# Kernel tuning notes

Measured on AMD Instinct MI355X. Metric: run time of the kernel, lower is better.

## Reference

```python
import jax, jax.numpy as jnp
import numpy as np

B, S, D, H, DFF = 2, 2048, 1024, 16, 4096
DK = D // H
EPS = 1e-5

def setup_inputs() -> dict:
    key = jax.random.key(0)
    ks = jax.random.split(key, 8)
    sc = lambda n: 1.0 / np.sqrt(n)
    return {
        "x": jax.random.normal(ks[0], (B, S, D), dtype=jnp.float32),
        "g1": jnp.ones((D,), dtype=jnp.float32),
        "g2": jnp.ones((D,), dtype=jnp.float32),
        "wq": jax.random.normal(ks[1], (D, D), dtype=jnp.float32) * sc(D),
        "wk": jax.random.normal(ks[2], (D, D), dtype=jnp.float32) * sc(D),
        "wv": jax.random.normal(ks[3], (D, D), dtype=jnp.float32) * sc(D),
        "wo": jax.random.normal(ks[4], (D, D), dtype=jnp.float32) * sc(D),
        "w1": jax.random.normal(ks[5], (DFF, D), dtype=jnp.float32) * sc(D),
        "w2": jax.random.normal(ks[6], (D, DFF), dtype=jnp.float32) * sc(DFF),
    }

def rmsnorm(a, g):
    norm = jnp.sqrt(jnp.mean(a * a, axis=-1, keepdims=True) + EPS)
    return a / norm * g

def gelu_erf(x):
    return x * 0.5 * (1.0 + jax.lax.erf(x * (1.0 / np.sqrt(2.0))))

def reference(x, g1, g2, wq, wk, wv, wo, w1, w2):
    b, s, d = x.shape
    h, dk = H, DK
    # --- attention sublayer (pre-norm) ---
    xn = rmsnorm(x, g1)
    # nn.Linear: y = x @ W.T ; reshape to [b, h, s, dk]
    q = (xn @ wq.T).reshape(b, s, h, dk).transpose(0, 2, 1, 3)
    k = (xn @ wk.T).reshape(b, s, h, dk).transpose(0, 2, 1, 3)
    v = (xn @ wv.T).reshape(b, s, h, dk).transpose(0, 2, 1, 3)
    scores = jnp.einsum('bhqd,bhkd->bhqk', q, k) / np.sqrt(dk).astype(np.float32)
    causal = jnp.triu(jnp.ones((s, s), dtype=bool), k=1)  # True above diagonal -> masked
    scores = jnp.where(causal, -jnp.inf, scores)
    weights = jax.nn.softmax(scores, axis=-1)
    attn = jnp.einsum('bhqk,bhkd->bhqd', weights, v)
    attn = attn.transpose(0, 2, 1, 3).reshape(b, s, d)
    x = x + attn @ wo.T
    # --- FFN sublayer (pre-norm) ---
    xn2 = rmsnorm(x, g2)
    ff = gelu_erf(xn2 @ w1.T) @ w2.T
    return x + ff
```

## Files before the change

### kernel.cpp

```cpp
#include <hip/hip_runtime.h>
#include <hip/hip_bf16.h>

typedef __attribute__((ext_vector_type(8))) short bf16x8;
typedef __attribute__((ext_vector_type(4))) float f32x4;

__device__ __forceinline__ unsigned short f2b(float f) {
    unsigned int u = __float_as_uint(f);
    unsigned int r = u + 0x7FFFu + ((u >> 16) & 1u);
    return (unsigned short)(r >> 16);
}

__device__ __forceinline__ float gelu_erf(float v) {
    return 0.5f * v * (1.0f + erff(v * 0.70710678118654752f));
}

__device__ __forceinline__ void gload_lds16(const void* g, void* l) {
    __builtin_amdgcn_global_load_lds(
        (const __attribute__((address_space(1))) void*)g,
        (__attribute__((address_space(3))) void*)l, 16, 0, 0);
}

__global__ void cast_all_k(const float* __restrict__ wq, const float* __restrict__ wk,
                           const float* __restrict__ wv, const float* __restrict__ wo,
                           const float* __restrict__ w1, const float* __restrict__ w2,
                           unsigned short* __restrict__ wqkv_b, unsigned short* __restrict__ wo_b,
                           unsigned short* __restrict__ w1_b, unsigned short* __restrict__ w2_b,
                           float qscale) {
    const int S = 262144, F = 1048576;
    int i = blockIdx.x * blockDim.x + threadIdx.x;
    const float* src; unsigned short* dst; int off; float scale = 1.0f;
    if (i < S)              { src = wq; dst = wqkv_b;             off = i;          scale = qscale; }
    else if (i < 2 * S)     { src = wk; dst = wqkv_b + S * 4;     off = i - S; }
    else if (i < 3 * S)     { src = wv; dst = wqkv_b + 2 * S * 4; off = i - 2 * S; }
    else if (i < 4 * S)     { src = wo; dst = wo_b;               off = i - 3 * S; }
    else if (i < 4 * S + F) { src = w1; dst = w1_b;               off = i - 4 * S; }
    else                    { src = w2; dst = w2_b;               off = i - 4 * S - F; }
    float4 v = ((const float4*)src)[off];
    ushort4 o;
    o.x = f2b(v.x * scale); o.y = f2b(v.y * scale);
    o.z = f2b(v.z * scale); o.w = f2b(v.w * scale);
    ((ushort4*)(dst))[off] = o;
}

__global__ void rmsnorm_bf16_k(const float* __restrict__ x, const float* __restrict__ g,
                               unsigned short* __restrict__ out) {
    int row = blockIdx.x;
    int t = threadIdx.x;
    const float4* xr = (const float4*)(x + (size_t)row * 1024);
    float4 xv = xr[t];
    float ss = xv.x * xv.x + xv.y * xv.y + xv.z * xv.z + xv.w * xv.w;
    #pragma unroll
    for (int off = 32; off; off >>= 1) ss += __shfl_xor(ss, off, 64);
    __shared__ float red[4];
    int wave = t >> 6, lane = t & 63;
    if (lane == 0) red[wave] = ss;
    __syncthreads();
    float tot = red[0] + red[1] + red[2] + red[3];
    float rn = rsqrtf(tot * (1.0f / 1024.0f) + 1e-5f);
    float4 gv = ((const float4*)g)[t];
    ushort4 o4;
    o4.x = f2b(xv.x * rn * gv.x);
    o4.y = f2b(xv.y * rn * gv.y);
    o4.z = f2b(xv.z * rn * gv.z);
    o4.w = f2b(xv.w * rn * gv.w);
    ((ushort4*)out)[(size_t)row * 256 + t] = o4;
}

__global__ void vtrans_k(const unsigned short* __restrict__ qkv, unsigned short* __restrict__ vt) {
    __shared__ unsigned short Ls[64 * 72];
    int st = blockIdx.x, bh = blockIdx.y, b = bh >> 4, h = bh & 15;
    int s0 = st * 64;
    int tid = threadIdx.x;
    const unsigned short* Vg = qkv + (size_t)(b * 2048 + s0) * 3072 + 2048 + h * 64;
    #pragma unroll
    for (int i = 0; i < 2; i++) {
        int idx = i * 256 + tid;
        int r = idx >> 3, c8 = (idx & 7) * 8;
        *(uint4*)&Ls[r * 72 + c8] = *(const uint4*)&Vg[(size_t)r * 3072 + c8];
    }
    __syncthreads();
    #pragma unroll
    for (int i = 0; i < 2; i++) {
        int idx = i * 256 + tid;
        int d = idx >> 3, s8 = (idx & 7) * 8;
        unsigned short tmp[8];
        #pragma unroll
        for (int j = 0; j < 8; j++) tmp[j] = Ls[(s8 + j) * 72 + d];
        *(uint4*)&vt[(size_t)(bh * 64 + d) * 2048 + s0 + s8] = *(uint4*)tmp;
    }
}

template <int EPI>
__launch_bounds__(256)
__global__ void gemm_bt(const unsigned short* __restrict__ A, const unsigned short* __restrict__ B,
                        const float* __restrict__ res, void* __restrict__ out,
                        int M, int N, int K) {
    __shared__ __align__(16) unsigned short smem[2 * 128 * 32];
    unsigned short* As = smem;
    unsigned short* Bs = smem + 128 * 32;

    int tid = threadIdx.x;
    int wave = tid >> 6, lane = tid & 63;
    int lrow = lane & 15, quad = lane >> 4;
    int qx8 = (quad ^ ((lrow >> 1) & 3)) * 8;

    int gx = gridDim.x, gy = gridDim.y;
    int cid = blockIdx.y * gx + blockIdx.x;
    int per = (gx * gy) >> 3;
    int nid = (cid & 7) * per + (cid >> 3);
    const int CG = 8;
    int group = nid / (CG * gy);
    int rem = nid % (CG * gy);
    int bxs = group * CG + (rem % CG);
    int bys = rem / CG;
    int bm = bys * 128, bn = bxs * 128;

    int wm = (wave & 1) * 64, wn = (wave >> 1) * 64;

    const unsigned short* Ab = A + (size_t)bm * K;
    const unsigned short* Bb = B + (size_t)bn * K;

    f32x4 zero = {0.f, 0.f, 0.f, 0.f};
    f32x4 acc[4][4];
    #pragma unroll
    for (int mi = 0; mi < 4; mi++)
        #pragma unroll
        for (int ni = 0; ni < 4; ni++) acc[mi][ni] = zero;

    int wbase = tid & 192;

    for (int k0 = 0; k0 < K; k0 += 32) {
        if (k0) __syncthreads();
        #pragma unroll
        for (int i = 0; i < 2; i++) {
            int idx = i * 256 + tid;
            int r = idx >> 2;
            int c = ((idx & 3) ^ ((idx >> 3) & 3)) * 8;
            gload_lds16(&Ab[(size_t)r * K + k0 + c], As + ((size_t)(i * 256 + wbase)) * 8);
            gload_lds16(&Bb[(size_t)r * K + k0 + c], Bs + ((size_t)(i * 256 + wbase)) * 8);
        }
        __syncthreads();

        bf16x8 af[4], bfr[4];
        #pragma unroll
        for (int mi = 0; mi < 4; mi++)
            af[mi] = *(const bf16x8*)&As[(wm + mi * 16 + lrow) * 32 + qx8];
        #pragma unroll
        for (int ni = 0; ni < 4; ni++)
            bfr[ni] = *(const bf16x8*)&Bs[(wn + ni * 16 + lrow) * 32 + qx8];
        #pragma unroll
        for (int mi = 0; mi < 4; mi++)
            #pragma unroll
            for (int ni = 0; ni < 4; ni++)
                acc[mi][ni] = __builtin_amdgcn_mfma_f32_16x16x32_bf16(af[mi], bfr[ni], acc[mi][ni], 0, 0, 0);
    }

    float* Cs = (float*)smem;
    int row16 = lane >> 2, cseg = (lane & 3) * 16;
    #pragma unroll
    for (int p = 0; p < 4; p++) {
        __syncthreads();
        #pragma unroll
        for (int ni = 0; ni < 4; ni++)
            #pragma unroll
            for (int r = 0; r < 4; r++)
                Cs[wave * 1024 + (quad * 4 + r) * 64 + ni * 16 + lrow] = acc[p][ni][r];
        __syncthreads();
        const float* src = &Cs[wave * 1024 + row16 * 64 + cseg];
        int grow = bm + wm + p * 16 + row16;
        int gcol = bn + wn + cseg;
        size_t off = (size_t)grow * N + gcol;
        if (EPI == 1) {
            float* op = (float*)out + off;
            const float* rp = res + off;
            #pragma unroll
            for (int j = 0; j < 4; j++) {
                float4 v = ((const float4*)src)[j];
                float4 rr = ((const float4*)rp)[j];
                v.x += rr.x; v.y += rr.y; v.z += rr.z; v.w += rr.w;
                ((float4*)op)[j] = v;
            }
        } else {
            unsigned short tmp[16];
            #pragma unroll
            for (int j = 0; j < 16; j++) {
                float v = src[j];
                if (EPI == 2) v = gelu_erf(v);
                tmp[j] = f2b(v);
            }
            unsigned short* op = (unsigned short*)out + off;
            *(uint4*)op = *(uint4*)tmp;
            *(uint4*)(op + 8) = *(uint4*)(tmp + 8);
        }
    }
}

__launch_bounds__(256)
__global__ void gemm_bt64(const unsigned short* __restrict__ A, const unsigned short* __restrict__ B,
                          const float* __restrict__ res, float* __restrict__ out,
                          int M, int N, int K) {
    __shared__ __align__(16) unsigned short As[2][128 * 32];
    __shared__ __align__(16) unsigned short Bs[2][64 * 32];

    int tid = threadIdx.x, wave = tid >> 6, lane = tid & 63;
    int lrow = lane & 15, quad = lane >> 4;
    int qx8 = (quad ^ ((lrow >> 1) & 3)) * 8;

    int gx = gridDim.x, gy = gridDim.y;
    int cid = blockIdx.y * gx + blockIdx.x;
    int per = (gx * gy) >> 3;
    int nid = (cid & 7) * per + (cid >> 3);
    const int CG = 8;
    int group = nid / (CG * gy);
    int rem = nid % (CG * gy);
    int bxs = group * CG + (rem % CG);
    int bys = rem / CG;
    int bm = bys * 128, bn = bxs * 64;

    int wm = (wave & 1) * 64, wn = (wave >> 1) * 32;

    f32x4 zero = {0.f, 0.f, 0.f, 0.f};
    f32x4 acc[4][2];
    #pragma unroll
    for (int mi = 0; mi < 4; mi++)
        #pragma unroll
        for (int ni = 0; ni < 2; ni++) acc[mi][ni] = zero;

    int rr4 = lane >> 2;
    int c8s = ((lane & 3) ^ ((lane >> 3) & 3)) * 8;
    const unsigned short* Ab = A + (size_t)(bm + wave * 32 + rr4) * K + c8s;
    const unsigned short* Bb = B + (size_t)(bn + wave * 16 + rr4) * K + c8s;

    auto stage = [&](int k0, int nb) {
        gload_lds16(Ab + k0, &As[nb][(wave * 32) * 32]);
        gload_lds16(Ab + (size_t)16 * K + k0, &As[nb][(wave * 32 + 16) * 32]);
        gload_lds16(Bb + k0, &Bs[nb][(wave * 16) * 32]);
    };

    int nIter = K >> 5;
    stage(0, 0);
    for (int it = 0; it < nIter; it++) {
        __syncthreads();
        if (it + 1 < nIter) stage((it + 1) * 32, (it + 1) & 1);
        int buf = it & 1;

        bf16x8 af[4], bfr[2];
        #pragma unroll
        for (int mi = 0; mi < 4; mi++)
            af[mi] = *(const bf16x8*)&As[buf][(wm + mi * 16 + lrow) * 32 + qx8];
        #pragma unroll
        for (int ni = 0; ni < 2; ni++)
            bfr[ni] = *(const bf16x8*)&Bs[buf][(wn + ni * 16 + lrow) * 32 + qx8];
        #pragma unroll
        for (int mi = 0; mi < 4; mi++)
            #pragma unroll
            for (int ni = 0; ni < 2; ni++)
                acc[mi][ni] = __builtin_amdgcn_mfma_f32_16x16x32_bf16(af[mi], bfr[ni], acc[mi][ni], 0, 0, 0);
    }

    float* Cs = (float*)As[0];
    int row16 = lane >> 2, cseg = (lane & 3) * 8;
    #pragma unroll
    for (int p = 0; p < 4; p++) {
        __syncthreads();
        #pragma unroll
        for (int ni = 0; ni < 2; ni++)
            #pragma unroll
            for (int r = 0; r < 4; r++)
                Cs[wave * 512 + (quad * 4 + r) * 32 + ni * 16 + lrow] = acc[p][ni][r];
        __syncthreads();
        const float* src = &Cs[wave * 512 + row16 * 32 + cseg];
        int grow = bm + wm + p * 16 + row16;
        int gcol = bn + wn + cseg;
        size_t off = (size_t)grow * N + gcol;
        float* op = out + off;
        const float* rp = res + off;
        #pragma unroll
        for (int j = 0; j < 2; j++) {
            float4 v = ((const float4*)src)[j];
            float4 rv = ((const float4*)rp)[j];
            v.x += rv.x; v.y += rv.y; v.z += rv.z; v.w += rv.w;
            ((float4*)op)[j] = v;
        }
    }
}

__launch_bounds__(256)
__global__ void attn_k(const unsigned short* __restrict__ qkv,
                       const unsigned short* __restrict__ vt,
                       unsigned short* __restrict__ attn_out) {
    const int ROWQKV = 3072;
    int cid = (int)(blockIdx.y * gridDim.x + blockIdx.x);
    int bh = (cid & 7) * 4 + (cid >> 6);
    int bx = (cid >> 3) & 7;
    int b = bh >> 4, h = bh & 15;
    int qtA = bx, qtB = 15 - bx;
    int nktA = 2 * qtA + 2, nktB = 2 * qtB + 2;
    int ntot = nktA + nktB;

    __shared__ __align__(16) unsigned short Ks[2][2][64 * 32];
    __shared__ __align__(16) unsigned short Vs[2][2][64 * 32];
    __shared__ __align__(16) unsigned short Ps[8][16 * 72];

    int tid = threadIdx.x, wave = tid >> 6, lane = tid & 63;
    int lrow = lane & 15, quad = lane >> 4;
    int rr4 = lane >> 2;
    int c8s = ((lane & 3) ^ ((lane >> 3) & 3)) * 8;
    int qx8 = (quad ^ ((lrow >> 1) & 3)) * 8;

    size_t base = (size_t)b * 2048 * ROWQKV;

    bf16x8 qf[2][2][2];
    #pragma unroll
    for (int p = 0; p < 2; p++) {
        int q0 = (p ? qtB : qtA) * 128;
        #pragma unroll
        for (int s = 0; s < 2; s++) {
            const unsigned short* Qg = qkv + base +
                (size_t)(q0 + s * 64 + wave * 16 + lrow) * ROWQKV + h * 64 + quad * 8;
            qf[p][s][0] = *(const bf16x8*)Qg;
            qf[p][s][1] = *(const bf16x8*)(Qg + 32);
        }
    }

    const unsigned short* Kg0 = qkv + base + (size_t)(wave * 16 + rr4) * ROWQKV + 1024 + h * 64 + c8s;
    const unsigned short* Vg0 = vt + (size_t)(bh * 64 + wave * 16 + rr4) * 2048 + c8s;

    auto stage = [&](int t, int nb) {
        const unsigned short* Kg = Kg0 + (size_t)(t * 64) * ROWQKV;
        const unsigned short* Vg = Vg0 + t * 64;
        gload_lds16(Kg,      &Ks[nb][0][wave * 16 * 32]);
        gload_lds16(Kg + 32, &Ks[nb][1][wave * 16 * 32]);
        gload_lds16(Vg,      &Vs[nb][0][wave * 16 * 32]);
        gload_lds16(Vg + 32, &Vs[nb][1][wave * 16 * 32]);
    };

    f32x4 zero = {0.f, 0.f, 0.f, 0.f};
    f32x4 oA[4], oB[4];
    float lA = 0.f, lB = 0.f;
    #pragma unroll
    for (int ni = 0; ni < 4; ni++) { oA[ni] = zero; oB[ni] = zero; }

    int qloc = wave * 16 + lrow;

    auto process = [&](bf16x8 q0f, bf16x8 q1f, f32x4* o, float& l,
                       unsigned short* Pw, bool diag, int buf) {
        f32x4 s[4];
        #pragma unroll
        for (int ni = 0; ni < 4; ni++) s[ni] = zero;
        #pragma unroll
        for (int ni = 0; ni < 4; ni++) {
            bf16x8 kf = *(const bf16x8*)&Ks[buf][0][(ni * 16 + lrow) * 32 + qx8];
            s[ni] = __builtin_amdgcn_mfma_f32_16x16x32_bf16(kf, q0f, s[ni], 0, 0, 0);
        }
        #pragma unroll
        for (int ni = 0; ni < 4; ni++) {
            bf16x8 kf = *(const bf16x8*)&Ks[buf][1][(ni * 16 + lrow) * 32 + qx8];
            s[ni] = __builtin_amdgcn_mfma_f32_16x16x32_bf16(kf, q1f, s[ni], 0, 0, 0);
        }
        if (diag) {
            #pragma unroll
            for (int ni = 0; ni < 4; ni++)
                #pragma unroll
                for (int r = 0; r < 4; r++) {
                    float p = exp2f(s[ni][r]);
                    if (ni * 16 + quad * 4 + r > qloc) p = 0.f;
                    s[ni][r] = p;
                    l += p;
                }
        } else {
            #pragma unroll
            for (int ni = 0; ni < 4; ni++)
                #pragma unroll
                for (int r = 0; r < 4; r++) {
                    float p = exp2f(s[ni][r]);
                    s[ni][r] = p;
                    l += p;
                }
        }
        #pragma unroll
        for (int ni = 0; ni < 4; ni++) {
            uint2 pk;
            pk.x = (unsigned int)f2b(s[ni][0]) | ((unsigned int)f2b(s[ni][1]) << 16);
            pk.y = (unsigned int)f2b(s[ni][2]) | ((unsigned int)f2b(s[ni][3]) << 16);
            *(uint2*)&Pw[lrow * 72 + ni * 16 + quad * 4] = pk;
        }
        bf16x8 p0 = *(const bf16x8*)&Pw[lrow * 72 + quad * 8];
        bf16x8 p1 = *(const bf16x8*)&Pw[lrow * 72 + 32 + quad * 8];
        #pragma unroll
        for (int ni = 0; ni < 4; ni++) {
            bf16x8 vf = *(const bf16x8*)&Vs[buf][0][(ni * 16 + lrow) * 32 + qx8];
            o[ni] = __builtin_amdgcn_mfma_f32_16x16x32_bf16(p0, vf, o[ni], 0, 0, 0);
        }
        #pragma unroll
        for (int ni = 0; ni < 4; ni++) {
            bf16x8 vf = *(const bf16x8*)&Vs[buf][1][(ni * 16 + lrow) * 32 + qx8];
            o[ni] = __builtin_amdgcn_mfma_f32_16x16x32_bf16(p1, vf, o[ni], 0, 0, 0);
        }
    };

    auto epilogue = [&](int qbase) {
        float la = lA, lb = lB;
        la += __shfl_xor(la, 16, 64); la += __shfl_xor(la, 32, 64);
        lb += __shfl_xor(lb, 16, 64); lb += __shfl_xor(lb, 32, 64);
        #pragma unroll
        for (int strip = 0; strip < 2; strip++) {
            f32x4* o = strip ? oB : oA;
            float lv = strip ? lb : la;
            #pragma unroll
            for (int r = 0; r < 4; r++) {
                float lr = __shfl(lv, quad * 4 + r, 64);
                float inv = 1.0f / lr;
                int q = qbase + strip * 64 + wave * 16 + quad * 4 + r;
                #pragma unroll
                for (int ni = 0; ni < 4; ni++)
                    attn_out[((size_t)b * 2048 + q) * 1024 + h * 64 + ni * 16 + lrow] =
                        f2b(o[ni][r] * inv);
            }
        }
    };

    stage(0, 0);

    for (int j = 0; j < ntot; j++) {
        __syncthreads();
        if (j + 1 < ntot) {
            int t = (j + 1 < nktA) ? (j + 1) : (j + 1 - nktA);
            stage(t, (j + 1) & 1);
        }
        int buf = j & 1;
        if (j < nktA) {
            if (j < nktA - 1)
                process(qf[0][0][0], qf[0][0][1], oA, lA, Ps[wave], j == nktA - 2, buf);
            process(qf[0][1][0], qf[0][1][1], oB, lB, Ps[wave + 4], j == nktA - 1, buf);
            if (j == nktA - 1) {
                epilogue(qtA * 128);
                #pragma unroll
                for (int ni = 0; ni < 4; ni++) { oA[ni] = zero; oB[ni] = zero; }
                lA = 0.f; lB = 0.f;
            }
        } else {
            int t = j - nktA;
            if (t < nktB - 1)
                process(qf[1][0][0], qf[1][0][1], oA, lA, Ps[wave], t == nktB - 2, buf);
            process(qf[1][1][0], qf[1][1][1], oB, lB, Ps[wave + 4], t == nktB - 1, buf);
        }
    }
    epilogue(qtB * 128);
}

extern "C" void kernel_launch(void* const* d_in, const int* in_sizes, int n_in,
                              void* d_out, int out_size, void* d_ws, size_t ws_size,
                              hipStream_t stream) {
    const float* x  = (const float*)d_in[0];
    const float* g1 = (const float*)d_in[1];
    const float* g2 = (const float*)d_in[2];
    const float* wq = (const float*)d_in[3];
    const float* wk = (const float*)d_in[4];
    const float* wv = (const float*)d_in[5];
    const float* wo = (const float*)d_in[6];
    const float* w1 = (const float*)d_in[7];
    const float* w2 = (const float*)d_in[8];
    float* out = (float*)d_out;

    const size_t BS = 4096;
    const size_t D = 1024, DFF = 4096;
    const float QSCALE = 0.18033688011112042f;

    char* w = (char*)d_ws;
    unsigned short* xn_b   = (unsigned short*)w; w += BS * D * 2;
    unsigned short* wqkv_b = (unsigned short*)w; w += 3 * D * D * 2;
    unsigned short* qkv_b  = (unsigned short*)w; w += BS * 3 * D * 2;
    unsigned short* vt_b   = (unsigned short*)w; w += BS * D * 2;
    unsigned short* attn_b = (unsigned short*)w; w += BS * D * 2;
    unsigned short* wo_b   = (unsigned short*)w; w += D * D * 2;
    float*          x2     = (float*)w;          w += BS * D * 4;
    unsigned short* xn2_b  = (unsigned short*)w; w += BS * D * 2;
    unsigned short* w1_b   = (unsigned short*)w; w += DFF * D * 2;
    unsigned short* h_b    = (unsigned short*)w; w += BS * DFF * 2;
    unsigned short* w2_b   = (unsigned short*)w; w += D * DFF * 2;

    cast_all_k<<<12288, 256, 0, stream>>>(wq, wk, wv, wo, w1, w2,
                                          wqkv_b, wo_b, w1_b, w2_b, QSCALE);

    rmsnorm_bf16_k<<<(int)BS, 256, 0, stream>>>(x, g1, xn_b);

    gemm_bt<0><<<dim3(24, 32), 256, 0, stream>>>(xn_b, wqkv_b, nullptr, qkv_b, 4096, 3072, 1024);

    vtrans_k<<<dim3(32, 32), 256, 0, stream>>>(qkv_b, vt_b);

    attn_k<<<dim3(8, 32), 256, 0, stream>>>(qkv_b, vt_b, attn_b);

    gemm_bt64<<<dim3(16, 32), 256, 0, stream>>>(attn_b, wo_b, x, x2, 4096, 1024, 1024);

    rmsnorm_bf16_k<<<(int)BS, 256, 0, stream>>>(x2, g2, xn2_b);

    gemm_bt<2><<<dim3(32, 32), 256, 0, stream>>>(xn2_b, w1_b, nullptr, h_b, 4096, 4096, 1024);

    gemm_bt64<<<dim3(16, 32), 256, 0, stream>>>(h_b, w2_b, x2, out, 4096, 1024, 4096);
}
```

Measured before the change: 373.6 us.

## Widen residual GEMM tiles to 128x128 with 64-deep K steps

Replaces the 128x64 residual-add GEMM used for the output projection and FFN down-projection with a 128x128 tile kernel that stages two 32-wide K slices per iteration. Each wave now computes a 64x64 sub-tile, which raises MFMA work per LDS load and halves the number of barriers per K. The block swizzle is simplified to a plain row-major remap after XCD interleaving. The trade-offs are more accumulator registers and LDS (64KB), and only 256 blocks for these GEMMs, which may leave compute units underfilled on a 256-CU part.

```diff
diff --git a/kernel.cpp b/kernel.cpp
--- a/kernel.cpp
+++ b/kernel.cpp
@@ -196,87 +196,93 @@
 }
 
 __launch_bounds__(256)
-__global__ void gemm_bt64(const unsigned short* __restrict__ A, const unsigned short* __restrict__ B,
-                          const float* __restrict__ res, float* __restrict__ out,
-                          int M, int N, int K) {
-    __shared__ __align__(16) unsigned short As[2][128 * 32];
-    __shared__ __align__(16) unsigned short Bs[2][64 * 32];
+__global__ void gemm_bt128(const unsigned short* __restrict__ A, const unsigned short* __restrict__ B,
+                           const float* __restrict__ res, float* __restrict__ out,
+                           int M, int N, int K) {
+    __shared__ __align__(16) unsigned short As[2][2][128 * 32];
+    __shared__ __align__(16) unsigned short Bs[2][2][128 * 32];
 
     int tid = threadIdx.x, wave = tid >> 6, lane = tid & 63;
     int lrow = lane & 15, quad = lane >> 4;
     int qx8 = (quad ^ ((lrow >> 1) & 3)) * 8;
+    int rr4 = lane >> 2;
+    int c8s = ((lane & 3) ^ ((lane >> 3) & 3)) * 8;
 
     int gx = gridDim.x, gy = gridDim.y;
     int cid = blockIdx.y * gx + blockIdx.x;
     int per = (gx * gy) >> 3;
     int nid = (cid & 7) * per + (cid >> 3);
-    const int CG = 8;
-    int group = nid / (CG * gy);
-    int rem = nid % (CG * gy);
-    int bxs = group * CG + (rem % CG);
-    int bys = rem / CG;
-    int bm = bys * 128, bn = bxs * 64;
-
-    int wm = (wave & 1) * 64, wn = (wave >> 1) * 32;
+    int bxs = nid % gx;
+    int bys = nid / gx;
+    int bm = bys * 128, bn = bxs * 128;
+
+    int wm = (wave & 1) * 64, wn = (wave >> 1) * 64;
+
+    const unsigned short* Ab = A + (size_t)(bm + wave * 32 + rr4) * K + c8s;
+    const unsigned short* Bb = B + (size_t)(bn + wave * 32 + rr4) * K + c8s;
 
     f32x4 zero = {0.f, 0.f, 0.f, 0.f};
-    f32x4 acc[4][2];
+    f32x4 acc[4][4];
     #pragma unroll
     for (int mi = 0; mi < 4; mi++)
         #pragma unroll
-        for (int ni = 0; ni < 2; ni++) acc[mi][ni] = zero;
-
-    int rr4 = lane >> 2;
-    int c8s = ((lane & 3) ^ ((lane >> 3) & 3)) * 8;
-    const unsigned short* Ab = A + (size_t)(bm + wave * 32 + rr4) * K + c8s;
-    const unsigned short* Bb = B + (size_t)(bn + wave * 16 + rr4) * K + c8s;
+        for (int ni = 0; ni < 4; ni++) acc[mi][ni] = zero;
 
     auto stage = [&](int k0, int nb) {
-        gload_lds16(Ab + k0, &As[nb][(wave * 32) * 32]);
-        gload_lds16(Ab + (size_t)16 * K + k0, &As[nb][(wave * 32 + 16) * 32]);
-        gload_lds16(Bb + k0, &Bs[nb][(wave * 16) * 32]);
+        #pragma unroll
+        for (int ks = 0; ks < 2; ks++) {
+            #pragma unroll
+            for (int hh = 0; hh < 2; hh++) {
+                gload_lds16(Ab + (size_t)(hh * 16) * K + k0 + ks * 32,
+                            &As[nb][ks][(wave * 32 + hh * 16) * 32]);
+                gload_lds16(Bb + (size_t)(hh * 16) * K + k0 + ks * 32,
+                            &Bs[nb][ks][(wave * 32 + hh * 16) * 32]);
+            }
+        }
     };
 
-    int nIter = K >> 5;
+    int nIter = K >> 6;
     stage(0, 0);
     for (int it = 0; it < nIter; it++) {
         __syncthreads();
-        if (it + 1 < nIter) stage((it + 1) * 32, (it + 1) & 1);
+        if (it + 1 < nIter) stage((it + 1) * 64, (it + 1) & 1);
         int buf = it & 1;
-
-        bf16x8 af[4], bfr[2];
-        #pragma unroll
-        for (int mi = 0; mi < 4; mi++)
-            af[mi] = *(const bf16x8*)&As[buf][(wm + mi * 16 + lrow) * 32 + qx8];
-        #pragma unroll
-        for (int ni = 0; ni < 2; ni++)
-            bfr[ni] = *(const bf16x8*)&Bs[buf][(wn + ni * 16 + lrow) * 32 + qx8];
-        #pragma unroll
-        for (int mi = 0; mi < 4; mi++)
-            #pragma unroll
-            for (int ni = 0; ni < 2; ni++)
-                acc[mi][ni] = __builtin_amdgcn_mfma_f32_16x16x32_bf16(af[mi], bfr[ni], acc[mi][ni], 0, 0, 0);
-    }
-
-    float* Cs = (float*)As[0];
-    int row16 = lane >> 2, cseg = (lane & 3) * 8;
+        #pragma unroll
+        for (int ks = 0; ks < 2; ks++) {
+            bf16x8 af[4], bfr[4];
+            #pragma unroll
+            for (int mi = 0; mi < 4; mi++)
+                af[mi] = *(const bf16x8*)&As[buf][ks][(wm + mi * 16 + lrow) * 32 + qx8];
+            #pragma unroll
+            for (int ni = 0; ni < 4; ni++)
+                bfr[ni] = *(const bf16x8*)&Bs[buf][ks][(wn + ni * 16 + lrow) * 32 + qx8];
+            #pragma unroll
+            for (int mi = 0; mi < 4; mi++)
+                #pragma unroll
+                for (int ni = 0; ni < 4; ni++)
+                    acc[mi][ni] = __builtin_amdgcn_mfma_f32_16x16x32_bf16(af[mi], bfr[ni], acc[mi][ni], 0, 0, 0);
+        }
+    }
+
+    float* Cs = (float*)&As[0][0][0];
+    int row16 = lane >> 2, cseg = (lane & 3) * 16;
     #pragma unroll
     for (int p = 0; p < 4; p++) {
         __syncthreads();
         #pragma unroll
-        for (int ni = 0; ni < 2; ni++)
+        for (int ni = 0; ni < 4; ni++)
             #pragma unroll
             for (int r = 0; r < 4; r++)
-                Cs[wave * 512 + (quad * 4 + r) * 32 + ni * 16 + lrow] = acc[p][ni][r];
-        __syncthreads();
-        const float* src = &Cs[wave * 512 + row16 * 32 + cseg];
+                Cs[wave * 1024 + (quad * 4 + r) * 64 + ni * 16 + lrow] = acc[p][ni][r];
+        __syncthreads();
+        const float* src = &Cs[wave * 1024 + row16 * 64 + cseg];
         int grow = bm + wm + p * 16 + row16;
         int gcol = bn + wn + cseg;
         size_t off = (size_t)grow * N + gcol;
         float* op = out + off;
         const float* rp = res + off;
         #pragma unroll
-        for (int j = 0; j < 2; j++) {
+        for (int j = 0; j < 4; j++) {
             float4 v = ((const float4*)src)[j];
             float4 rv = ((const float4*)rp)[j];
             v.x += rv.x; v.y += rv.y; v.z += rv.z; v.w += rv.w;
@@ -491,11 +497,11 @@
 
     attn_k<<<dim3(8, 32), 256, 0, stream>>>(qkv_b, vt_b, attn_b);
 
-    gemm_bt64<<<dim3(16, 32), 256, 0, stream>>>(attn_b, wo_b, x, x2, 4096, 1024, 1024);
+    gemm_bt128<<<dim3(8, 32), 256, 0, stream>>>(attn_b, wo_b, x, x2, 4096, 1024, 1024);
 
     rmsnorm_bf16_k<<<(int)BS, 256, 0, stream>>>(x2, g2, xn2_b);
 
     gemm_bt<2><<<dim3(32, 32), 256, 0, stream>>>(xn2_b, w1_b, nullptr, h_b, 4096, 4096, 1024);
 
-    gemm_bt64<<<dim3(16, 32), 256, 0, stream>>>(h_b, w2_b, x2, out, 4096, 1024, 4096);
-}
+    gemm_bt128<<<dim3(8, 32), 256, 0, stream>>>(h_b, w2_b, x2, out, 4096, 1024, 4096);
+}
```

After: 377.5 us. Within noise of the previous version (+1.0%).

## Replace N=64 output GEMMs with split-K atomic-accumulate GEMMs seeded by rmsnorm copies

Applied to the files above, without the earlier changes.

The two output-projection GEMMs (Wo and W2) now use the 128x128 gemm_bt tile with split-K over blockIdx.z. Each partial result is atomically added into an fp32 output buffer, and the separate gemm_bt64 kernel is removed. The residual is pre-seeded by having each rmsnorm kernel write a copy of its input row into the destination buffer, so the GEMM epilogue no longer reads the residual. This increases grid parallelism for these narrow N=1024 GEMMs but adds fp32 atomic traffic, makes the summation order nondeterministic, and drops the double-buffered pipeline that gemm_bt64 had.

```diff
diff --git a/kernel.cpp b/kernel.cpp
--- a/kernel.cpp
+++ b/kernel.cpp
@@ -43,7 +43,7 @@
 }
 
 __global__ void rmsnorm_bf16_k(const float* __restrict__ x, const float* __restrict__ g,
-                               unsigned short* __restrict__ out) {
+                               unsigned short* __restrict__ out, float* __restrict__ copy) {
     int row = blockIdx.x;
     int t = threadIdx.x;
     const float4* xr = (const float4*)(x + (size_t)row * 1024);
@@ -54,6 +54,7 @@
     __shared__ float red[4];
     int wave = t >> 6, lane = t & 63;
     if (lane == 0) red[wave] = ss;
+    if (copy) ((float4*)copy)[(size_t)row * 256 + t] = xv;
     __syncthreads();
     float tot = red[0] + red[1] + red[2] + red[3];
     float rn = rsqrtf(tot * (1.0f / 1024.0f) + 1e-5f);
@@ -94,7 +95,7 @@
 __launch_bounds__(256)
 __global__ void gemm_bt(const unsigned short* __restrict__ A, const unsigned short* __restrict__ B,
                         const float* __restrict__ res, void* __restrict__ out,
-                        int M, int N, int K) {
+                        int M, int N, int K, int Kchunk) {
     __shared__ __align__(16) unsigned short smem[2 * 128 * 32];
     unsigned short* As = smem;
     unsigned short* Bs = smem + 128 * 32;
@@ -115,6 +116,8 @@
     int bys = rem / CG;
     int bm = bys * 128, bn = bxs * 128;
 
+    int kbase = (int)blockIdx.z * Kchunk;
+
     int wm = (wave & 1) * 64, wn = (wave >> 1) * 64;
 
     const unsigned short* Ab = A + (size_t)bm * K;
@@ -129,8 +132,9 @@
 
     int wbase = tid & 192;
 
-    for (int k0 = 0; k0 < K; k0 += 32) {
-        if (k0) __syncthreads();
+    for (int kk = 0; kk < Kchunk; kk += 32) {
+        int k0 = kbase + kk;
+        if (kk) __syncthreads();
         #pragma unroll
         for (int i = 0; i < 2; i++) {
             int idx = i * 256 + tid;
@@ -153,6 +157,21 @@
             #pragma unroll
             for (int ni = 0; ni < 4; ni++)
                 acc[mi][ni] = __builtin_amdgcn_mfma_f32_16x16x32_bf16(af[mi], bfr[ni], acc[mi][ni], 0, 0, 0);
+    }
+
+    if (EPI == 3) {
+        float* op = (float*)out;
+        #pragma unroll
+        for (int mi = 0; mi < 4; mi++)
+            #pragma unroll
+            for (int r = 0; r < 4; r++) {
+                int row = bm + wm + mi * 16 + quad * 4 + r;
+                size_t rowoff = (size_t)row * N + bn + wn;
+                #pragma unroll
+                for (int ni = 0; ni < 4; ni++)
+                    atomicAdd(&op[rowoff + ni * 16 + lrow], acc[mi][ni][r]);
+            }
+        return;
     }
 
     float* Cs = (float*)smem;
@@ -191,96 +210,6 @@
             unsigned short* op = (unsigned short*)out + off;
             *(uint4*)op = *(uint4*)tmp;
             *(uint4*)(op + 8) = *(uint4*)(tmp + 8);
-        }
-    }
-}
-
-__launch_bounds__(256)
-__global__ void gemm_bt64(const unsigned short* __restrict__ A, const unsigned short* __restrict__ B,
-                          const float* __restrict__ res, float* __restrict__ out,
-                          int M, int N, int K) {
-    __shared__ __align__(16) unsigned short As[2][128 * 32];
-    __shared__ __align__(16) unsigned short Bs[2][64 * 32];
-
-    int tid = threadIdx.x, wave = tid >> 6, lane = tid & 63;
-    int lrow = lane & 15, quad = lane >> 4;
-    int qx8 = (quad ^ ((lrow >> 1) & 3)) * 8;
-
-    int gx = gridDim.x, gy = gridDim.y;
-    int cid = blockIdx.y * gx + blockIdx.x;
-    int per = (gx * gy) >> 3;
-    int nid = (cid & 7) * per + (cid >> 3);
-    const int CG = 8;
-    int group = nid / (CG * gy);
-    int rem = nid % (CG * gy);
-    int bxs = group * CG + (rem % CG);
-    int bys = rem / CG;
-    int bm = bys * 128, bn = bxs * 64;
-
-    int wm = (wave & 1) * 64, wn = (wave >> 1) * 32;
-
-    f32x4 zero = {0.f, 0.f, 0.f, 0.f};
-    f32x4 acc[4][2];
-    #pragma unroll
-    for (int mi = 0; mi < 4; mi++)
-        #pragma unroll
-        for (int ni = 0; ni < 2; ni++) acc[mi][ni] = zero;
-
-    int rr4 = lane >> 2;
-    int c8s = ((lane & 3) ^ ((lane >> 3) & 3)) * 8;
-    const unsigned short* Ab = A + (size_t)(bm + wave * 32 + rr4) * K + c8s;
-    const unsigned short* Bb = B + (size_t)(bn + wave * 16 + rr4) * K + c8s;
-
-    auto stage = [&](int k0, int nb) {
-        gload_lds16(Ab + k0, &As[nb][(wave * 32) * 32]);
-        gload_lds16(Ab + (size_t)16 * K + k0, &As[nb][(wave * 32 + 16) * 32]);
-        gload_lds16(Bb + k0, &Bs[nb][(wave * 16) * 32]);
-    };
-
-    int nIter = K >> 5;
-    stage(0, 0);
-    for (int it = 0; it < nIter; it++) {
-        __syncthreads();
-        if (it + 1 < nIter) stage((it + 1) * 32, (it + 1) & 1);
-        int buf = it & 1;
-
-        bf16x8 af[4], bfr[2];
-        #pragma unroll
-        for (int mi = 0; mi < 4; mi++)
-            af[mi] = *(const bf16x8*)&As[buf][(wm + mi * 16 + lrow) * 32 + qx8];
-        #pragma unroll
-        for (int ni = 0; ni < 2; ni++)
-            bfr[ni] = *(const bf16x8*)&Bs[buf][(wn + ni * 16 + lrow) * 32 + qx8];
-        #pragma unroll
-        for (int mi = 0; mi < 4; mi++)
-            #pragma unroll
-            for (int ni = 0; ni < 2; ni++)
-                acc[mi][ni] = __builtin_amdgcn_mfma_f32_16x16x32_bf16(af[mi], bfr[ni], acc[mi][ni], 0, 0, 0);
-    }
-
-    float* Cs = (float*)As[0];
-    int row16 = lane >> 2, cseg = (lane & 3) * 8;
-    #pragma unroll
-    for (int p = 0; p < 4; p++) {
-        __syncthreads();
-        #pragma unroll
-        for (int ni = 0; ni < 2; ni++)
-            #pragma unroll
-            for (int r = 0; r < 4; r++)
-                Cs[wave * 512 + (quad * 4 + r) * 32 + ni * 16 + lrow] = acc[p][ni][r];
-        __syncthreads();
-        const float* src = &Cs[wave * 512 + row16 * 32 + cseg];
-        int grow = bm + wm + p * 16 + row16;
-        int gcol = bn + wn + cseg;
-        size_t off = (size_t)grow * N + gcol;
-        float* op = out + off;
-        const float* rp = res + off;
-        #pragma unroll
-        for (int j = 0; j < 2; j++) {
-            float4 v = ((const float4*)src)[j];
-            float4 rv = ((const float4*)rp)[j];
-            v.x += rv.x; v.y += rv.y; v.z += rv.z; v.w += rv.w;
-            ((float4*)op)[j] = v;
         }
     }
 }
@@ -483,19 +412,19 @@
     cast_all_k<<<12288, 256, 0, stream>>>(wq, wk, wv, wo, w1, w2,
                                           wqkv_b, wo_b, w1_b, w2_b, QSCALE);
 
-    rmsnorm_bf16_k<<<(int)BS, 256, 0, stream>>>(x, g1, xn_b);
-
-    gemm_bt<0><<<dim3(24, 32), 256, 0, stream>>>(xn_b, wqkv_b, nullptr, qkv_b, 4096, 3072, 1024);
+    rmsnorm_bf16_k<<<(int)BS, 256, 0, stream>>>(x, g1, xn_b, x2);
+
+    gemm_bt<0><<<dim3(24, 32), 256, 0, stream>>>(xn_b, wqkv_b, nullptr, qkv_b, 4096, 3072, 1024, 1024);
 
     vtrans_k<<<dim3(32, 32), 256, 0, stream>>>(qkv_b, vt_b);
 
     attn_k<<<dim3(8, 32), 256, 0, stream>>>(qkv_b, vt_b, attn_b);
 
-    gemm_bt64<<<dim3(16, 32), 256, 0, stream>>>(attn_b, wo_b, x, x2, 4096, 1024, 1024);
-
-    rmsnorm_bf16_k<<<(int)BS, 256, 0, stream>>>(x2, g2, xn2_b);
-
-    gemm_bt<2><<<dim3(32, 32), 256, 0, stream>>>(xn2_b, w1_b, nullptr, h_b, 4096, 4096, 1024);
-
-    gemm_bt64<<<dim3(16, 32), 256, 0, stream>>>(h_b, w2_b, x2, out, 4096, 1024, 4096);
-}
+    gemm_bt<3><<<dim3(8, 32, 2), 256, 0, stream>>>(attn_b, wo_b, nullptr, x2, 4096, 1024, 1024, 512);
+
+    rmsnorm_bf16_k<<<(int)BS, 256, 0, stream>>>(x2, g2, xn2_b, out);
+
+    gemm_bt<2><<<dim3(32, 32), 256, 0, stream>>>(xn2_b, w1_b, nullptr, h_b, 4096, 4096, 1024, 1024);
+
+    gemm_bt<3><<<dim3(8, 32, 4), 256, 0, stream>>>(h_b, w2_b, nullptr, out, 4096, 1024, 4096, 1024);
+}
```

New measurement: 403.3 us. 7.9% more time.
